# Kernel tuning notes

Measured on AMD Instinct MI355X. Metric: run time of the kernel, lower is better.

The kernel has to match this reference:

```python
import jax, jax.numpy as jnp
import numpy as np
import math

NUM_V = 32; NUM_K = 16; DK = 128; DV = 128; KCONV = 4; H = 2048
KEY_DIM = NUM_K * DK          # 2048
VALUE_DIM = NUM_V * DV        # 4096
CONV_DIM = 2 * KEY_DIM + VALUE_DIM  # 8192
EPS = 1e-6
VPK = NUM_V // NUM_K


def setup_inputs() -> dict:
    key = jax.random.key(0)
    ks = jax.random.split(key, 12)
    s = 0.02  # weight scale for numerical sanity
    return {
        "hidden_in": jax.random.normal(ks[0], (1, 1, H), jnp.float32),
        "conv_state": jax.random.normal(ks[1], (1, CONV_DIM, KCONV), jnp.float32),
        "rec_state": jax.random.normal(ks[2], (1, NUM_V, DK, DV), jnp.float32) * s,
        "W_qkv": jax.random.normal(ks[3], (CONV_DIM, H), jnp.float32) * s,
        "W_z": jax.random.normal(ks[4], (VALUE_DIM, H), jnp.float32) * s,
        "W_b": jax.random.normal(ks[5], (NUM_V, H), jnp.float32) * s,
        "W_a": jax.random.normal(ks[6], (NUM_V, H), jnp.float32) * s,
        "W_out": jax.random.normal(ks[7], (H, VALUE_DIM), jnp.float32) * s,
        "conv_w": jax.random.normal(ks[8], (CONV_DIM, KCONV), jnp.float32) * s,
        "dt_bias": jax.random.normal(ks[9], (NUM_V,), jnp.float32),
        "A_log": jax.random.normal(ks[10], (NUM_V,), jnp.float32),
        "norm_w": jnp.ones((DV,), jnp.float32),
    }


def _l2norm(x, eps=1e-6):
    return x * jax.lax.rsqrt(jnp.sum(x * x, axis=-1, keepdims=True) + eps)


def reference(hidden_in, conv_state, rec_state, W_qkv, W_z, W_b, W_a,
              W_out, conv_w, dt_bias, A_log, norm_w):
    h = hidden_in[0, 0]                       # (H,)
    mixed = W_qkv @ h                         # (CONV_DIM,)
    z = W_z @ h                               # (VALUE_DIM,)
    b = W_b @ h                               # (NUM_V,)
    a = W_a @ h                               # (NUM_V,)

    # causal conv1d update: shift state by one, take dot with kernel
    w = jnp.concatenate([conv_state, mixed[None, :, None]], axis=-1)  # (1, C, K+1)
    new_conv_state = w[:, :, 1:]                                      # (1, C, K)
    conv_out = jax.nn.silu(jnp.sum(new_conv_state * conv_w[None], axis=-1))[0]  # (C,)

    q = conv_out[:KEY_DIM].reshape(NUM_K, DK)
    k = conv_out[KEY_DIM:2 * KEY_DIM].reshape(NUM_K, DK)
    v = conv_out[2 * KEY_DIM:].reshape(NUM_V, DV)
    q = jnp.repeat(q, VPK, axis=0)            # (NUM_V, DK)
    k = jnp.repeat(k, VPK, axis=0)

    q = _l2norm(q) * (1.0 / math.sqrt(DK))
    k = _l2norm(k)

    beta = jax.nn.sigmoid(b)                                  # (NUM_V,)
    g = -jnp.exp(A_log) * jax.nn.softplus(a + dt_bias)        # (NUM_V,)

    # gated delta-rule recurrent update
    rec = rec_state[0] * jnp.exp(g)[:, None, None]            # (NUM_V, DK, DV)
    kv_mem = jnp.einsum('hkd,hk->hd', rec, k)                 # (NUM_V, DV)
    delta = (v - kv_mem) * beta[:, None]
    rec = rec + k[:, :, None] * delta[:, None, :]
    core = jnp.einsum('hkd,hk->hd', rec, q)                   # (NUM_V, DV)

    # gated RMSNorm over Dv per head
    var = jnp.mean(core * core, axis=-1, keepdims=True)
    xn = core * jax.lax.rsqrt(var + EPS) * norm_w
    zf = z.reshape(NUM_V, DV)
    out = (xn * jax.nn.silu(zf)).reshape(VALUE_DIM)

    hidden_out = (W_out @ out).reshape(1, 1, H)
    return (hidden_out, new_conv_state, rec[None])
```

## Files before the change

### kernel.cpp

```cpp
#include <hip/hip_runtime.h>

#define HDIM 2048
#define NUM_V 32
#define NUM_K 16
#define DK 128
#define DV 128
#define KEY_DIM 2048
#define VALUE_DIM 4096
#define CONV_DIM 8192
#define TOTAL_ROWS 12352



__global__ __launch_bounds__(256) void k1_gemv(
    const float* __restrict__ h,
    const float* __restrict__ Wqkv,
    const float* __restrict__ Wz,
    const float* __restrict__ Wb,
    const float* __restrict__ Wa,
    const float* __restrict__ conv_state,
    const float* __restrict__ conv_w,
    float* __restrict__ ws,
    float* __restrict__ out_conv)
{
    const int row  = (blockIdx.x * 256 + threadIdx.x) >> 6;
    const int lane = threadIdx.x & 63;
    if (row >= TOTAL_ROWS) return;

    const float* wrow;
    if (row < 8192)       wrow = Wqkv + (size_t)row * HDIM;
    else if (row < 12288) wrow = Wz   + (size_t)(row - 8192) * HDIM;
    else if (row < 12320) wrow = Wb   + (size_t)(row - 12288) * HDIM;
    else                  wrow = Wa   + (size_t)(row - 12320) * HDIM;

    float acc = 0.f;
#pragma unroll
    for (int i = 0; i < 8; ++i) {
        const int idx = (i * 64 + lane) * 4;
        float4 w4 = *reinterpret_cast<const float4*>(wrow + idx);
        float4 h4 = *reinterpret_cast<const float4*>(h + idx);
        acc += w4.x * h4.x + w4.y * h4.y + w4.z * h4.z + w4.w * h4.w;
    }
#pragma unroll
    for (int off = 32; off > 0; off >>= 1)
        acc += __shfl_down(acc, off, 64);

    if (lane == 0) {
        if (row < 8192) {
            float4 cs = *reinterpret_cast<const float4*>(conv_state + row * 4);
            float4 cw = *reinterpret_cast<const float4*>(conv_w + row * 4);
            float pre = cs.y * cw.x + cs.z * cw.y + cs.w * cw.z + acc * cw.w;
            float co = pre / (1.f + expf(-pre));
            ws[row] = co;
            float4 ncs;
            ncs.x = cs.y; ncs.y = cs.z; ncs.z = cs.w; ncs.w = acc;
            *reinterpret_cast<float4*>(out_conv + row * 4) = ncs;
        } else {
            ws[row] = acc;
        }
    }
}

__global__ __launch_bounds__(1024) void k2_rec(
    const float* __restrict__ ws,
    const float* __restrict__ rec_in,
    const float* __restrict__ dt_bias,
    const float* __restrict__ A_log,
    const float* __restrict__ norm_w,
    float* __restrict__ rec_out,
    float* __restrict__ out_vec)
{
    __shared__ float s_k[128];
    __shared__ float s_q[128];
    __shared__ float s_delta[128];
    __shared__ float s_part[8][128];
    __shared__ float s_red[4];

    const int hh  = blockIdx.x;
    const int t   = threadIdx.x;
    const int d   = t & 127;
    const int kkb = t >> 7;
    const int kh  = hh >> 1;

    const float bv    = ws[12288 + hh];
    const float av    = ws[12320 + hh];
    const float beta  = 1.f / (1.f + expf(-bv));
    const float x     = av + dt_bias[hh];
    const float sp    = fmaxf(x, 0.f) + log1pf(expf(-fabsf(x)));
    const float decay = expf(-expf(A_log[hh]) * sp);

    float qr = 0.f, kr = 0.f;
    if (t < 128) {
        qr = ws[kh * 128 + d];
        kr = ws[KEY_DIM + kh * 128 + d];
        float sq = qr * qr, sk = kr * kr;
#pragma unroll
        for (int off = 32; off > 0; off >>= 1) {
            sq += __shfl_down(sq, off, 64);
            sk += __shfl_down(sk, off, 64);
        }
        if ((t & 63) == 0) { s_red[t >> 6] = sq; s_red[2 + (t >> 6)] = sk; }
    }
    __syncthreads();
    if (t < 128) {
        const float ssq = s_red[0] + s_red[1];
        const float ssk = s_red[2] + s_red[3];
        s_q[d] = qr * rsqrtf(ssq + 1e-6f) * 0.08838834764831845f;
        s_k[d] = kr * rsqrtf(ssk + 1e-6f);
    }
    __syncthreads();

    const float* rrow = rec_in  + (size_t)hh * (DK * DV) + kkb * 16 * DV;
    float*       wrow = rec_out + (size_t)hh * (DK * DV) + kkb * 16 * DV;

    float kvp = 0.f;
#pragma unroll
    for (int i = 0; i < 16; ++i)
        kvp += rrow[i * DV + d] * s_k[kkb * 16 + i];
    s_part[kkb][d] = kvp;
    __syncthreads();

    if (t < 128) {
        float kv = 0.f;
#pragma unroll
        for (int j = 0; j < 8; ++j) kv += s_part[j][d];
        kv *= decay;
        const float vv = ws[2 * KEY_DIM + hh * 128 + d];
        s_delta[d] = (vv - kv) * beta;
    }
    __syncthreads();

    const float dlt = s_delta[d];
    float corep = 0.f;
#pragma unroll
    for (int i = 0; i < 16; ++i) {
        const float r = rrow[i * DV + d] * decay + s_k[kkb * 16 + i] * dlt;
        wrow[i * DV + d] = r;
        corep += r * s_q[kkb * 16 + i];
    }
    s_part[kkb][d] = corep;
    __syncthreads();

    float core = 0.f;
    if (t < 128) {
#pragma unroll
        for (int j = 0; j < 8; ++j) core += s_part[j][d];
        float sc = core * core;
#pragma unroll
        for (int off = 32; off > 0; off >>= 1)
            sc += __shfl_down(sc, off, 64);
        if ((t & 63) == 0) s_red[t >> 6] = sc;
    }
    __syncthreads();
    if (t < 128) {
        const float ssc = s_red[0] + s_red[1];
        const float xn  = core * rsqrtf(ssc * (1.f / 128.f) + 1e-6f) * norm_w[d];
        const float zv  = ws[8192 + hh * 128 + d];
        out_vec[hh * 128 + d] = xn * (zv / (1.f + expf(-zv)));
    }
}

__global__ __launch_bounds__(256) void k3_out(
    const float* __restrict__ Wout,
    const float* __restrict__ out_vec,
    float* __restrict__ hidden_out)
{
    const int row  = (blockIdx.x * 256 + threadIdx.x) >> 6;
    const int lane = threadIdx.x & 63;
    if (row >= HDIM) return;

    const float* wrow = Wout + (size_t)row * VALUE_DIM;
    float acc = 0.f;
#pragma unroll
    for (int i = 0; i < 16; ++i) {
        const int idx = (i * 64 + lane) * 4;
        float4 w4 = *reinterpret_cast<const float4*>(wrow + idx);
        float4 o4 = *reinterpret_cast<const float4*>(out_vec + idx);
        acc += w4.x * o4.x + w4.y * o4.y + w4.z * o4.z + w4.w * o4.w;
    }
#pragma unroll
    for (int off = 32; off > 0; off >>= 1)
        acc += __shfl_down(acc, off, 64);
    if (lane == 0) hidden_out[row] = acc;
}

extern "C" void kernel_launch(void* const* d_in, const int* in_sizes, int n_in,
                              void* d_out, int out_size, void* d_ws, size_t ws_size,
                              hipStream_t stream) {
    const float* hidden_in  = (const float*)d_in[0];
    const float* conv_state = (const float*)d_in[1];
    const float* rec_state  = (const float*)d_in[2];
    const float* W_qkv      = (const float*)d_in[3];
    const float* W_z        = (const float*)d_in[4];
    const float* W_b        = (const float*)d_in[5];
    const float* W_a        = (const float*)d_in[6];
    const float* W_out      = (const float*)d_in[7];
    const float* conv_w     = (const float*)d_in[8];
    const float* dt_bias    = (const float*)d_in[9];
    const float* A_log      = (const float*)d_in[10];
    const float* norm_w     = (const float*)d_in[11];

    float* out = (float*)d_out;
    float* ws  = (float*)d_ws;

    k1_gemv<<<TOTAL_ROWS / 4, 256, 0, stream>>>(hidden_in, W_qkv, W_z, W_b, W_a,
                                                conv_state, conv_w, ws, out + 2048);
    k2_rec<<<NUM_V, 1024, 0, stream>>>(ws, rec_state, dt_bias, A_log, norm_w,
                                       out + 2048 + CONV_DIM * 4, ws + 12352);
    k3_out<<<HDIM / 4, 256, 0, stream>>>(W_out, ws + 12352, out);
}
```

Before: 32.67 us.

## Fuse three kernels into one cooperative persistent kernel with grid syncs

```diff
diff --git a/kernel.cpp b/kernel.cpp
--- a/kernel.cpp
+++ b/kernel.cpp
@@ -1,4 +1,7 @@
 #include <hip/hip_runtime.h>
+#include <hip/hip_cooperative_groups.h>
+
+namespace cg = cooperative_groups;
 
 #define HDIM 2048
 #define NUM_V 32
@@ -12,176 +15,177 @@
 
 
 
-__global__ __launch_bounds__(256) void k1_gemv(
+typedef __attribute__((ext_vector_type(4))) float f32x4;
+
+__global__ __launch_bounds__(512, 4) void fused(
     const float* __restrict__ h,
     const float* __restrict__ Wqkv,
     const float* __restrict__ Wz,
     const float* __restrict__ Wb,
     const float* __restrict__ Wa,
+    const float* __restrict__ Wout,
     const float* __restrict__ conv_state,
     const float* __restrict__ conv_w,
-    float* __restrict__ ws,
-    float* __restrict__ out_conv)
-{
-    const int row  = (blockIdx.x * 256 + threadIdx.x) >> 6;
-    const int lane = threadIdx.x & 63;
-    if (row >= TOTAL_ROWS) return;
-
-    const float* wrow;
-    if (row < 8192)       wrow = Wqkv + (size_t)row * HDIM;
-    else if (row < 12288) wrow = Wz   + (size_t)(row - 8192) * HDIM;
-    else if (row < 12320) wrow = Wb   + (size_t)(row - 12288) * HDIM;
-    else                  wrow = Wa   + (size_t)(row - 12320) * HDIM;
-
-    float acc = 0.f;
-#pragma unroll
-    for (int i = 0; i < 8; ++i) {
-        const int idx = (i * 64 + lane) * 4;
-        float4 w4 = *reinterpret_cast<const float4*>(wrow + idx);
-        float4 h4 = *reinterpret_cast<const float4*>(h + idx);
-        acc += w4.x * h4.x + w4.y * h4.y + w4.z * h4.z + w4.w * h4.w;
-    }
-#pragma unroll
-    for (int off = 32; off > 0; off >>= 1)
-        acc += __shfl_down(acc, off, 64);
-
-    if (lane == 0) {
-        if (row < 8192) {
-            float4 cs = *reinterpret_cast<const float4*>(conv_state + row * 4);
-            float4 cw = *reinterpret_cast<const float4*>(conv_w + row * 4);
-            float pre = cs.y * cw.x + cs.z * cw.y + cs.w * cw.z + acc * cw.w;
-            float co = pre / (1.f + expf(-pre));
-            ws[row] = co;
-            float4 ncs;
-            ncs.x = cs.y; ncs.y = cs.z; ncs.z = cs.w; ncs.w = acc;
-            *reinterpret_cast<float4*>(out_conv + row * 4) = ncs;
-        } else {
-            ws[row] = acc;
-        }
-    }
-}
-
-__global__ __launch_bounds__(1024) void k2_rec(
-    const float* __restrict__ ws,
     const float* __restrict__ rec_in,
     const float* __restrict__ dt_bias,
     const float* __restrict__ A_log,
     const float* __restrict__ norm_w,
-    float* __restrict__ rec_out,
-    float* __restrict__ out_vec)
+    float* __restrict__ ws,
+    float* __restrict__ out)
 {
+    cg::grid_group grid = cg::this_grid();
+
+    const int t      = threadIdx.x;
+    const int lane   = t & 63;
+    const int wid    = t >> 6;
+    const int gwave  = blockIdx.x * 8 + wid;
+    const int nwaves = gridDim.x * 8;
+
+    float* out_vec    = ws + 12352;
+    float* hidden_out = out;
+    float* new_conv   = out + 2048;
+    float* rec_out    = out + 2048 + CONV_DIM * 4;
+
+    for (int row = gwave; row < TOTAL_ROWS; row += nwaves) {
+        const float* wrow;
+        if (row < 8192)       wrow = Wqkv + (size_t)row * HDIM;
+        else if (row < 12288) wrow = Wz   + (size_t)(row - 8192) * HDIM;
+        else if (row < 12320) wrow = Wb   + (size_t)(row - 12288) * HDIM;
+        else                  wrow = Wa   + (size_t)(row - 12320) * HDIM;
+
+        float acc = 0.f;
+#pragma unroll
+        for (int i = 0; i < 8; ++i) {
+            const int idx = (i * 64 + lane) * 4;
+            f32x4 w4 = *reinterpret_cast<const f32x4*>(wrow + idx);
+            f32x4 h4 = *reinterpret_cast<const f32x4*>(h + idx);
+            acc += w4.x * h4.x + w4.y * h4.y + w4.z * h4.z + w4.w * h4.w;
+        }
+#pragma unroll
+        for (int off = 32; off > 0; off >>= 1)
+            acc += __shfl_down(acc, off, 64);
+
+        if (lane == 0) {
+            if (row < 8192) {
+                f32x4 cs = *reinterpret_cast<const f32x4*>(conv_state + row * 4);
+                f32x4 cw = *reinterpret_cast<const f32x4*>(conv_w + row * 4);
+                float pre = cs.y * cw.x + cs.z * cw.y + cs.w * cw.z + acc * cw.w;
+                ws[row] = pre / (1.f + expf(-pre));
+                f32x4 n; n.x = cs.y; n.y = cs.z; n.z = cs.w; n.w = acc;
+                *reinterpret_cast<f32x4*>(new_conv + row * 4) = n;
+            } else {
+                ws[row] = acc;
+            }
+        }
+    }
+
+    grid.sync();
+
     __shared__ float s_k[128];
     __shared__ float s_q[128];
     __shared__ float s_delta[128];
-    __shared__ float s_part[8][128];
+    __shared__ float s_part[4][128];
     __shared__ float s_red[4];
 
-    const int hh  = blockIdx.x;
-    const int t   = threadIdx.x;
-    const int d   = t & 127;
-    const int kkb = t >> 7;
-    const int kh  = hh >> 1;
-
-    const float bv    = ws[12288 + hh];
-    const float av    = ws[12320 + hh];
-    const float beta  = 1.f / (1.f + expf(-bv));
-    const float x     = av + dt_bias[hh];
-    const float sp    = fmaxf(x, 0.f) + log1pf(expf(-fabsf(x)));
-    const float decay = expf(-expf(A_log[hh]) * sp);
-
-    float qr = 0.f, kr = 0.f;
-    if (t < 128) {
-        qr = ws[kh * 128 + d];
-        kr = ws[KEY_DIM + kh * 128 + d];
-        float sq = qr * qr, sk = kr * kr;
-#pragma unroll
-        for (int off = 32; off > 0; off >>= 1) {
-            sq += __shfl_down(sq, off, 64);
-            sk += __shfl_down(sk, off, 64);
-        }
-        if ((t & 63) == 0) { s_red[t >> 6] = sq; s_red[2 + (t >> 6)] = sk; }
+    for (int hh = blockIdx.x; hh < NUM_V; hh += gridDim.x) {
+        const int d   = t & 127;
+        const int kkb = t >> 7;
+        const int kh  = hh >> 1;
+
+        const float bv    = ws[12288 + hh];
+        const float av    = ws[12320 + hh];
+        const float beta  = 1.f / (1.f + expf(-bv));
+        const float x     = av + dt_bias[hh];
+        const float sp    = fmaxf(x, 0.f) + log1pf(expf(-fabsf(x)));
+        const float decay = expf(-expf(A_log[hh]) * sp);
+
+        float qr = 0.f, kr = 0.f;
+        if (t < 128) {
+            qr = ws[kh * 128 + d];
+            kr = ws[KEY_DIM + kh * 128 + d];
+            float sq = qr * qr, sk = kr * kr;
+#pragma unroll
+            for (int off = 32; off > 0; off >>= 1) {
+                sq += __shfl_down(sq, off, 64);
+                sk += __shfl_down(sk, off, 64);
+            }
+            if ((t & 63) == 0) { s_red[t >> 6] = sq; s_red[2 + (t >> 6)] = sk; }
+        }
+        __syncthreads();
+        if (t < 128) {
+            const float ssq = s_red[0] + s_red[1];
+            const float ssk = s_red[2] + s_red[3];
+            s_q[d] = qr * rsqrtf(ssq + 1e-6f) * 0.08838834764831845f;
+            s_k[d] = kr * rsqrtf(ssk + 1e-6f);
+        }
+        __syncthreads();
+
+        const float* rrow = rec_in  + (size_t)hh * (DK * DV) + kkb * 32 * DV;
+        float*       wrow = rec_out + (size_t)hh * (DK * DV) + kkb * 32 * DV;
+
+        float kvp = 0.f;
+#pragma unroll 8
+        for (int i = 0; i < 32; ++i)
+            kvp += rrow[i * DV + d] * s_k[kkb * 32 + i];
+        s_part[kkb][d] = kvp;
+        __syncthreads();
+
+        if (t < 128) {
+            float kv = (s_part[0][d] + s_part[1][d]) + (s_part[2][d] + s_part[3][d]);
+            kv *= decay;
+            const float vv = ws[2 * KEY_DIM + hh * 128 + d];
+            s_delta[d] = (vv - kv) * beta;
+        }
+        __syncthreads();
+
+        const float dlt = s_delta[d];
+        float corep = 0.f;
+#pragma unroll 8
+        for (int i = 0; i < 32; ++i) {
+            const float r = rrow[i * DV + d] * decay + s_k[kkb * 32 + i] * dlt;
+            wrow[i * DV + d] = r;
+            corep += r * s_q[kkb * 32 + i];
+        }
+        s_part[kkb][d] = corep;
+        __syncthreads();
+
+        if (t < 128) {
+            const float core = (s_part[0][d] + s_part[1][d]) + (s_part[2][d] + s_part[3][d]);
+            float sc = core * core;
+#pragma unroll
+            for (int off = 32; off > 0; off >>= 1)
+                sc += __shfl_down(sc, off, 64);
+            if ((t & 63) == 0) s_red[t >> 6] = sc;
+            s_delta[d] = core;
+        }
+        __syncthreads();
+        if (t < 128) {
+            const float core = s_delta[d];
+            const float ssc  = s_red[0] + s_red[1];
+            const float xn   = core * rsqrtf(ssc * (1.f / 128.f) + 1e-6f) * norm_w[d];
+            const float zv   = ws[8192 + hh * 128 + d];
+            out_vec[hh * 128 + d] = xn * (zv / (1.f + expf(-zv)));
+        }
+        __syncthreads();
     }
-    __syncthreads();
-    if (t < 128) {
-        const float ssq = s_red[0] + s_red[1];
-        const float ssk = s_red[2] + s_red[3];
-        s_q[d] = qr * rsqrtf(ssq + 1e-6f) * 0.08838834764831845f;
-        s_k[d] = kr * rsqrtf(ssk + 1e-6f);
+
+    grid.sync();
+
+    for (int row = gwave; row < HDIM; row += nwaves) {
+        const float* wrow = Wout + (size_t)row * VALUE_DIM;
+        float acc = 0.f;
+#pragma unroll
+        for (int i = 0; i < 16; ++i) {
+            const int idx = (i * 64 + lane) * 4;
+            f32x4 w4 = *reinterpret_cast<const f32x4*>(wrow + idx);
+            f32x4 o4 = *reinterpret_cast<const f32x4*>(out_vec + idx);
+            acc += w4.x * o4.x + w4.y * o4.y + w4.z * o4.z + w4.w * o4.w;
+        }
+#pragma unroll
+        for (int off = 32; off > 0; off >>= 1)
+            acc += __shfl_down(acc, off, 64);
+        if (lane == 0) hidden_out[row] = acc;
     }
-    __syncthreads();
-
-    const float* rrow = rec_in  + (size_t)hh * (DK * DV) + kkb * 16 * DV;
-    float*       wrow = rec_out + (size_t)hh * (DK * DV) + kkb * 16 * DV;
-
-    float kvp = 0.f;
-#pragma unroll
-    for (int i = 0; i < 16; ++i)
-        kvp += rrow[i * DV + d] * s_k[kkb * 16 + i];
-    s_part[kkb][d] = kvp;
-    __syncthreads();
-
-    if (t < 128) {
-        float kv = 0.f;
-#pragma unroll
-        for (int j = 0; j < 8; ++j) kv += s_part[j][d];
-        kv *= decay;
-        const float vv = ws[2 * KEY_DIM + hh * 128 + d];
-        s_delta[d] = (vv - kv) * beta;
-    }
-    __syncthreads();
-
-    const float dlt = s_delta[d];
-    float corep = 0.f;
-#pragma unroll
-    for (int i = 0; i < 16; ++i) {
-        const float r = rrow[i * DV + d] * decay + s_k[kkb * 16 + i] * dlt;
-        wrow[i * DV + d] = r;
-        corep += r * s_q[kkb * 16 + i];
-    }
-    s_part[kkb][d] = corep;
-    __syncthreads();
-
-    float core = 0.f;
-    if (t < 128) {
-#pragma unroll
-        for (int j = 0; j < 8; ++j) core += s_part[j][d];
-        float sc = core * core;
-#pragma unroll
-        for (int off = 32; off > 0; off >>= 1)
-            sc += __shfl_down(sc, off, 64);
-        if ((t & 63) == 0) s_red[t >> 6] = sc;
-    }
-    __syncthreads();
-    if (t < 128) {
-        const float ssc = s_red[0] + s_red[1];
-        const float xn  = core * rsqrtf(ssc * (1.f / 128.f) + 1e-6f) * norm_w[d];
-        const float zv  = ws[8192 + hh * 128 + d];
-        out_vec[hh * 128 + d] = xn * (zv / (1.f + expf(-zv)));
-    }
-}
-
-__global__ __launch_bounds__(256) void k3_out(
-    const float* __restrict__ Wout,
-    const float* __restrict__ out_vec,
-    float* __restrict__ hidden_out)
-{
-    const int row  = (blockIdx.x * 256 + threadIdx.x) >> 6;
-    const int lane = threadIdx.x & 63;
-    if (row >= HDIM) return;
-
-    const float* wrow = Wout + (size_t)row * VALUE_DIM;
-    float acc = 0.f;
-#pragma unroll
-    for (int i = 0; i < 16; ++i) {
-        const int idx = (i * 64 + lane) * 4;
-        float4 w4 = *reinterpret_cast<const float4*>(wrow + idx);
-        float4 o4 = *reinterpret_cast<const float4*>(out_vec + idx);
-        acc += w4.x * o4.x + w4.y * o4.y + w4.z * o4.z + w4.w * o4.w;
-    }
-#pragma unroll
-    for (int off = 32; off > 0; off >>= 1)
-        acc += __shfl_down(acc, off, 64);
-    if (lane == 0) hidden_out[row] = acc;
 }
 
 extern "C" void kernel_launch(void* const* d_in, const int* in_sizes, int n_in,
@@ -203,9 +207,17 @@
     float* out = (float*)d_out;
     float* ws  = (float*)d_ws;
 
-    k1_gemv<<<TOTAL_ROWS / 4, 256, 0, stream>>>(hidden_in, W_qkv, W_z, W_b, W_a,
-                                                conv_state, conv_w, ws, out + 2048);
-    k2_rec<<<NUM_V, 1024, 0, stream>>>(ws, rec_state, dt_bias, A_log, norm_w,
-                                       out + 2048 + CONV_DIM * 4, ws + 12352);
-    k3_out<<<HDIM / 4, 256, 0, stream>>>(W_out, ws + 12352, out);
+    int maxb = 0;
+    if (hipOccupancyMaxActiveBlocksPerMultiprocessor(&maxb, fused, 512, 0) != hipSuccess
+        || maxb < 1)
+        maxb = 1;
+    int grid = maxb * 256;
+    if (grid > 512) grid = 512;
+
+    void* args[] = {
+        (void*)&hidden_in, (void*)&W_qkv, (void*)&W_z, (void*)&W_b, (void*)&W_a,
+        (void*)&W_out, (void*)&conv_state, (void*)&conv_w, (void*)&rec_state,
+        (void*)&dt_bias, (void*)&A_log, (void*)&norm_w, (void*)&ws, (void*)&out
+    };
+    hipLaunchCooperativeKernel((void*)fused, dim3(grid), dim3(512), args, 0, stream);
 }
```

Result: slower. 98.33 us (+201.0%).
